# Optimization experiments

Hardware: AMD Instinct MI355X
Metric: run time of the kernel (lower is better)

Reference implementation:

```python
import jax, jax.numpy as jnp
import numpy as np

BIG = 1e9
GRAPH_LAYERS = 2
FLOW_ITERS = 10
DUAL_ITERS = 10
STEP = 0.1
MOM = 0.9


def _forward(node_features, node_embeddings, demands, adj, neighborhoods,
             enc_W0, enc_b0, enc_W1, enc_b1,
             attn_W, attn_a_src, attn_a_dst, nbr_q,
             gru_W, gru_U, gru_b,
             dec_W0, dec_b0, dec_W1, dec_b1,
             dual_W0, dual_b0, dual_W1, dual_b1):
    E = enc_W1.shape[1]
    K = neighborhoods.shape[0]
    # --- node encoder MLP (tanh, activate_final=True) ---
    x = jnp.concatenate([node_embeddings, node_features], axis=-1)  # [B,N,Fin]
    h = jnp.tanh(jnp.tanh(x @ enc_W0 + enc_b0) @ enc_W1 + enc_b1)   # [B,N,E]
    attn_coefs = None
    for _ in range(GRAPH_LAYERS):
        # --- AttentionNeighborhood: multi-head GAT per hop level, then attention over levels ---
        z = jnp.einsum('bnd,hde->hbne', h, attn_W)                   # [H,B,N,E]
        s_src = jnp.einsum('hbne,he->hbn', z, attn_a_src)
        s_dst = jnp.einsum('hbne,he->hbn', z, attn_a_dst)
        scores = jnp.tanh(s_src[:, :, :, None] + s_dst[:, :, None, :])  # [H,B,N,N]
        aggs = []
        for k in range(K):
            masked = jnp.where(neighborhoods[k][None] > 0, scores, -BIG)
            alpha = jax.nn.softmax(masked, axis=-1)                  # [H,B,N,N]
            agg = jnp.tanh(jnp.einsum('hbnm,hbme->hbne', alpha, z).mean(axis=0))  # heads averaged -> [B,N,E]
            aggs.append(agg)
        aggs = jnp.stack(aggs, axis=2)                               # [B,N,K,E]
        attn_coefs = jax.nn.softmax(jnp.tanh(jnp.einsum('bnke,e->bnk', aggs, nbr_q)), axis=-1)
        nxt = jnp.einsum('bnk,bnke->bne', attn_coefs, aggs)          # [B,N,E]
        # --- GRU state update (tanh activation) ---
        zr = jax.nn.sigmoid(nxt @ gru_W[:, :2 * E] + h @ gru_U[:, :2 * E] + gru_b[:2 * E])
        zg, r = zr[..., :E], zr[..., E:]
        h_tilde = jnp.tanh(nxt @ gru_W[:, 2 * E:] + (r * h) @ gru_U[:, 2 * E:] + gru_b[2 * E:])
        h = (1.0 - zg) * h + zg * h_tilde
    # --- flow-proportion decoder + masked softmax over neighbors ---
    node_weights = jnp.tanh(h @ dec_W0 + dec_b0) @ dec_W1 + dec_b1   # [B,N,1]
    pred = adj * jnp.swapaxes(node_weights, 1, 2)                    # adj * node_weights^T
    weights = -BIG * (1.0 - adj) + pred
    prop = jax.nn.softmax(weights, axis=-1)                          # [B,N,N]
    # --- iterative min-cost-flow solver ---
    def mcf_step(flow, _):
        inflow = flow.sum(axis=1)[:, :, None]                        # inflow_i = sum_j flow[j,i]
        return prop * jax.nn.relu(inflow - demands), None
    flow, _ = jax.lax.scan(mcf_step, jnp.zeros_like(prop), None, length=FLOW_ITERS)
    # should_correct_flows: cancel opposing flow on each edge pair
    flow = flow - adj * jnp.minimum(flow, jnp.swapaxes(flow, 1, 2))
    flow_cost = jnp.sum(flow * flow, axis=(1, 2))                    # square cost, per graph
    # --- dual decoder + projected momentum ascent dual-flow solver ---
    dual_vars = jnp.tanh(h @ dual_W0 + dual_b0) @ dual_W1 + dual_b1  # [B,N,1]
    dual_diff = adj * (dual_vars - jnp.swapaxes(dual_vars, 1, 2))    # [B,N,N]
    def dual_step(carry, _):
        y, m = carry
        g = 2.0 * y - dual_diff                                      # d/dy [y^2 - dual_diff*y]
        m = MOM * m + g
        y = adj * jax.nn.relu(y - STEP * m)
        return (y, m), None
    (dflow, _m), _ = jax.lax.scan(dual_step,
                                  (jnp.zeros_like(dual_diff), jnp.zeros_like(dual_diff)),
                                  None, length=DUAL_ITERS)
    dual_demand = jnp.sum(dual_vars * demands, axis=(1, 2))
    dual_cost = jnp.sum(dflow * dflow - dual_diff * dflow, axis=(1, 2)) - dual_demand
    return flow_cost - dual_cost                                     # primal-dual gap loss, [B]


def setup_inputs() -> dict:
    key = jax.random.key(0)
    ks = jax.random.split(key, 24)
    B, N, Femb, Ffeat, E, H = 2, 2048, 16, 2, 64, 2
    Fin = Femb + Ffeat
    node_embeddings = jax.random.normal(ks[0], (B, N, Femb), jnp.float32)
    node_features = jax.random.normal(ks[1], (B, N, Ffeat), jnp.float32)
    d = jax.random.normal(ks[2], (B, N, 1), jnp.float32) * 0.1
    demands = d - d.mean(axis=1, keepdims=True)                      # balanced demands
    eye = jnp.eye(N, dtype=jnp.float32)
    u = jax.random.uniform(ks[3], (B, N, N))
    adj = (u < 0.008).astype(jnp.float32) * (1.0 - eye)              # avg degree ~16
    a2 = (jnp.matmul(adj, adj) > 0).astype(jnp.float32) * (1.0 - eye)
    neighborhoods = jnp.stack([adj, a2], axis=0)                     # [K,B,N,N]
    def init(k, fan_in, shape):
        return jax.random.normal(k, shape, jnp.float32) / jnp.sqrt(float(fan_in))
    return {
        'node_features': node_features, 'node_embeddings': node_embeddings,
        'demands': demands, 'adj': adj, 'neighborhoods': neighborhoods,
        'enc_W0': init(ks[4], Fin, (Fin, 64)), 'enc_b0': jnp.zeros((64,)),
        'enc_W1': init(ks[5], 64, (64, E)), 'enc_b1': jnp.zeros((E,)),
        'attn_W': init(ks[6], E, (H, E, E)),
        'attn_a_src': init(ks[7], E, (H, E)), 'attn_a_dst': init(ks[8], E, (H, E)),
        'nbr_q': init(ks[9], E, (E,)),
        'gru_W': init(ks[10], E, (E, 3 * E)), 'gru_U': init(ks[11], E, (E, 3 * E)),
        'gru_b': jnp.zeros((3 * E,)),
        'dec_W0': init(ks[12], E, (E, 64)), 'dec_b0': jnp.zeros((64,)),
        'dec_W1': init(ks[13], 64, (64, 1)), 'dec_b1': jnp.zeros((1,)),
        'dual_W0': init(ks[14], E, (E, 64)), 'dual_b0': jnp.zeros((64,)),
        'dual_W1': init(ks[15], 64, (64, 1)), 'dual_b1': jnp.zeros((1,)),
    }


def reference(node_features, node_embeddings, demands, adj, neighborhoods,
              enc_W0, enc_b0, enc_W1, enc_b1,
              attn_W, attn_a_src, attn_a_dst, nbr_q,
              gru_W, gru_U, gru_b,
              dec_W0, dec_b0, dec_W1, dec_b1,
              dual_W0, dual_b0, dual_W1, dual_b1):
    return _forward(node_features, node_embeddings, demands, adj, neighborhoods,
                    enc_W0, enc_b0, enc_W1, enc_b1,
                    attn_W, attn_a_src, attn_a_dst, nbr_q,
                    gru_W, gru_U, gru_b,
                    dec_W0, dec_b0, dec_W1, dec_b1,
                    dual_W0, dual_b0, dual_W1, dual_b1)
```

## Files before the change

kernel.cpp:

```cpp
#include <hip/hip_runtime.h>

#define B_ 2
#define N_ 2048
#define E_ 64
#define FIN_ 18
#define ADJ_CAP 128
#define A2_CAP 1024
#define ROWS 8

__device__ __forceinline__ float wave_sum(float v) {
  #pragma unroll
  for (int o = 32; o > 0; o >>= 1) v += __shfl_xor(v, o);
  return v;
}
__device__ __forceinline__ float wave_max(float v) {
  #pragma unroll
  for (int o = 32; o > 0; o >>= 1) v = fmaxf(v, __shfl_xor(v, o));
  return v;
}

__global__ void k_zero(int* __restrict__ tcnt, float* __restrict__ accum) {
  int i = blockIdx.x * 256 + threadIdx.x;
  if (i < B_ * N_) tcnt[i] = 0;
  if (i < 8) accum[i] = 0.f;
}

__global__ void k_csr(const float* __restrict__ nbhd, int* __restrict__ adj_idx,
                      int* __restrict__ adj_cnt, int* __restrict__ a2_idx,
                      int* __restrict__ a2_cnt) {
  int wid = blockIdx.x * 4 + (threadIdx.x >> 6);
  int lane = threadIdx.x & 63;
  int k = wid / (B_ * N_);
  int rem = wid - k * (B_ * N_);
  const float* row = nbhd + ((size_t)k * (B_ * N_) + rem) * N_;
  int cap = (k == 0) ? ADJ_CAP : A2_CAP;
  int* idx = ((k == 0) ? adj_idx : a2_idx) + (size_t)rem * cap;
  int* cntp = ((k == 0) ? adj_cnt : a2_cnt) + rem;
  int cnt = 0;
  for (int j0 = 0; j0 < N_; j0 += 64) {
    float v = row[j0 + lane];
    bool p = v > 0.f;
    unsigned long long m = __ballot(p);
    int pre = __popcll(m & ((1ull << lane) - 1ull));
    if (p) { int pos = cnt + pre; if (pos < cap) idx[pos] = j0 + lane; }
    cnt += __popcll(m);
  }
  if (lane == 0) *cntp = (cnt < cap) ? cnt : cap;
}

__global__ void k_enc(const float* __restrict__ emb, const float* __restrict__ feat,
                      const float* __restrict__ W0, const float* __restrict__ b0,
                      const float* __restrict__ W1, const float* __restrict__ b1,
                      float* __restrict__ h) {
  int j = threadIdx.x;
  int row0 = blockIdx.x * ROWS;
  __shared__ float X[ROWS][FIN_];
  __shared__ float HID[ROWS][64];
  for (int t = j; t < ROWS * FIN_; t += 64) {
    int r = t / FIN_, d = t % FIN_;
    int row = row0 + r;
    X[r][d] = (d < 16) ? emb[(size_t)row * 16 + d] : feat[(size_t)row * 2 + (d - 16)];
  }
  __syncthreads();
  float acc[ROWS];
  #pragma unroll
  for (int r = 0; r < ROWS; r++) acc[r] = b0[j];
  for (int d = 0; d < FIN_; d++) {
    float w = W0[d * 64 + j];
    #pragma unroll
    for (int r = 0; r < ROWS; r++) acc[r] += X[r][d] * w;
  }
  #pragma unroll
  for (int r = 0; r < ROWS; r++) HID[r][j] = tanhf(acc[r]);
  __syncthreads();
  float acc2[ROWS];
  #pragma unroll
  for (int r = 0; r < ROWS; r++) acc2[r] = b1[j];
  for (int d = 0; d < 64; d++) {
    float w = W1[d * 64 + j];
    #pragma unroll
    for (int r = 0; r < ROWS; r++) acc2[r] += HID[r][d] * w;
  }
  #pragma unroll
  for (int r = 0; r < ROWS; r++) h[(size_t)(row0 + r) * 64 + j] = tanhf(acc2[r]);
}

__global__ void k_z(const float* __restrict__ h, const float* __restrict__ attn_W,
                    const float* __restrict__ a_src, const float* __restrict__ a_dst,
                    float* __restrict__ z, float* __restrict__ ssrc, float* __restrict__ sdst) {
  int tid = threadIdx.x;
  int head = tid >> 6, j = tid & 63;
  int row0 = blockIdx.x * ROWS;
  __shared__ float HR[ROWS][64];
  for (int t = tid; t < ROWS * 64; t += 128) HR[t >> 6][t & 63] = h[(size_t)row0 * 64 + t];
  __syncthreads();
  float acc[ROWS];
  #pragma unroll
  for (int r = 0; r < ROWS; r++) acc[r] = 0.f;
  const float* W = attn_W + head * 64 * 64;
  for (int d = 0; d < 64; d++) {
    float w = W[d * 64 + j];
    #pragma unroll
    for (int r = 0; r < ROWS; r++) acc[r] += HR[r][d] * w;
  }
  float as = a_src[head * 64 + j], ad = a_dst[head * 64 + j];
  #pragma unroll
  for (int r = 0; r < ROWS; r++) {
    float zv = acc[r];
    z[((size_t)head * (B_ * N_) + row0 + r) * 64 + j] = zv;
    float rs = wave_sum(zv * as);
    float rd = wave_sum(zv * ad);
    if (j == 0) {
      ssrc[head * (B_ * N_) + row0 + r] = rs;
      sdst[head * (B_ * N_) + row0 + r] = rd;
    }
  }
}

__global__ void k_agg(const int* __restrict__ adj_idx, const int* __restrict__ adj_cnt,
                      const int* __restrict__ a2_idx, const int* __restrict__ a2_cnt,
                      const float* __restrict__ z, const float* __restrict__ ssrc,
                      const float* __restrict__ sdst, float* __restrict__ aggs) {
  int k = blockIdx.x & 1;
  int row = blockIdx.x >> 1;
  int tid = threadIdx.x;
  int w = tid >> 6, lane = tid & 63;
  int b = row >> 11;
  int cap = (k == 0) ? ADJ_CAP : A2_CAP;
  const int* idx = ((k == 0) ? adj_idx : a2_idx) + (size_t)row * cap;
  int cnt = ((k == 0) ? adj_cnt : a2_cnt)[row];
  __shared__ float SC0[A2_CAP], SC1[A2_CAP];
  __shared__ int COL[A2_CAP];
  __shared__ float WS[4][64];
  __shared__ float RED[2][4];
  float ss0 = ssrc[row], ss1 = ssrc[B_ * N_ + row];
  const float* sd0 = sdst + b * N_;
  const float* sd1 = sdst + B_ * N_ + b * N_;
  float sum0 = 0.f, sum1 = 0.f;
  for (int t = tid; t < cnt; t += 256) {
    int c = idx[t];
    COL[t] = c;
    float e0 = __expf(tanhf(ss0 + sd0[c]));
    float e1 = __expf(tanhf(ss1 + sd1[c]));
    SC0[t] = e0; SC1[t] = e1;
    sum0 += e0; sum1 += e1;
  }
  sum0 = wave_sum(sum0); sum1 = wave_sum(sum1);
  if (lane == 0) { RED[0][w] = sum0; RED[1][w] = sum1; }
  __syncthreads();
  float tot0 = RED[0][0] + RED[0][1] + RED[0][2] + RED[0][3];
  float tot1 = RED[1][0] + RED[1][1] + RED[1][2] + RED[1][3];
  float inv0 = (tot0 > 0.f) ? 1.f / tot0 : 0.f;
  float inv1 = (tot1 > 0.f) ? 1.f / tot1 : 0.f;
  const float* z0 = z + ((size_t)b * N_) * 64;
  const float* z1 = z + ((size_t)(B_ * N_) + b * N_) * 64;
  int g = lane >> 4, li = lane & 15;
  float4 a0 = {0.f, 0.f, 0.f, 0.f}, a1 = {0.f, 0.f, 0.f, 0.f};
  for (int base = w * 4; base < cnt; base += 16) {
    int t = base + g;
    if (t < cnt) {
      int c = COL[t];
      float e0 = SC0[t], e1 = SC1[t];
      float4 v0 = ((const float4*)(z0 + (size_t)c * 64))[li];
      float4 v1 = ((const float4*)(z1 + (size_t)c * 64))[li];
      a0.x += e0 * v0.x; a0.y += e0 * v0.y; a0.z += e0 * v0.z; a0.w += e0 * v0.w;
      a1.x += e1 * v1.x; a1.y += e1 * v1.y; a1.z += e1 * v1.z; a1.w += e1 * v1.w;
    }
  }
  #pragma unroll
  for (int o = 16; o <= 32; o <<= 1) {
    a0.x += __shfl_xor(a0.x, o); a0.y += __shfl_xor(a0.y, o);
    a0.z += __shfl_xor(a0.z, o); a0.w += __shfl_xor(a0.w, o);
    a1.x += __shfl_xor(a1.x, o); a1.y += __shfl_xor(a1.y, o);
    a1.z += __shfl_xor(a1.z, o); a1.w += __shfl_xor(a1.w, o);
  }
  if (g == 0) {
    WS[w][li * 4 + 0] = a0.x * inv0 + a1.x * inv1;
    WS[w][li * 4 + 1] = a0.y * inv0 + a1.y * inv1;
    WS[w][li * 4 + 2] = a0.z * inv0 + a1.z * inv1;
    WS[w][li * 4 + 3] = a0.w * inv0 + a1.w * inv1;
  }
  __syncthreads();
  if (tid < 64) {
    float s = WS[0][tid] + WS[1][tid] + WS[2][tid] + WS[3][tid];
    aggs[((size_t)row * 2 + k) * 64 + tid] = tanhf(0.5f * s);
  }
}

__global__ void k_comb(const float* __restrict__ aggs, const float* __restrict__ nbr_q,
                       const float* __restrict__ gru_W, const float* __restrict__ gru_U,
                       const float* __restrict__ gru_b, float* __restrict__ h) {
  int tid = threadIdx.x;
  int w = tid >> 6, j = tid & 63;
  int row0 = blockIdx.x * ROWS;
  __shared__ float NXT[ROWS][64], HROW[ROWS][64], RG[ROWS][64], ZG[ROWS][64];
  for (int t = tid; t < ROWS * 64; t += 128) HROW[t >> 6][t & 63] = h[(size_t)row0 * 64 + t];
  float q = nbr_q[j];
  for (int r = w * (ROWS / 2); r < (w + 1) * (ROWS / 2); r++) {
    float a0 = aggs[((size_t)(row0 + r) * 2 + 0) * 64 + j];
    float a1 = aggs[((size_t)(row0 + r) * 2 + 1) * 64 + j];
    float t0 = tanhf(wave_sum(a0 * q));
    float t1 = tanhf(wave_sum(a1 * q));
    float mx = fmaxf(t0, t1);
    float e0 = __expf(t0 - mx), e1 = __expf(t1 - mx);
    float inv = 1.f / (e0 + e1);
    NXT[r][j] = (e0 * a0 + e1 * a1) * inv;
  }
  __syncthreads();
  {
    float acc[ROWS];
    #pragma unroll
    for (int r = 0; r < ROWS; r++) acc[r] = gru_b[tid];
    for (int d = 0; d < 64; d++) {
      float wW = gru_W[d * 192 + tid];
      float wU = gru_U[d * 192 + tid];
      #pragma unroll
      for (int r = 0; r < ROWS; r++) acc[r] += NXT[r][d] * wW + HROW[r][d] * wU;
    }
    #pragma unroll
    for (int r = 0; r < ROWS; r++) {
      float zr = 1.f / (1.f + __expf(-acc[r]));
      if (tid < 64) ZG[r][tid] = zr; else RG[r][tid - 64] = zr;
    }
  }
  __syncthreads();
  if (tid < 64) {
    int col = 128 + tid;
    float acc[ROWS];
    #pragma unroll
    for (int r = 0; r < ROWS; r++) acc[r] = gru_b[col];
    for (int d = 0; d < 64; d++) {
      float wW = gru_W[d * 192 + col];
      float wU = gru_U[d * 192 + col];
      #pragma unroll
      for (int r = 0; r < ROWS; r++) acc[r] += NXT[r][d] * wW + (RG[r][d] * HROW[r][d]) * wU;
    }
    #pragma unroll
    for (int r = 0; r < ROWS; r++) {
      float ht = tanhf(acc[r]);
      float zg = ZG[r][tid];
      h[(size_t)(row0 + r) * 64 + tid] = (1.f - zg) * HROW[r][tid] + zg * ht;
    }
  }
}

__global__ void k_dec(const float* __restrict__ h, const float* __restrict__ dW0,
                      const float* __restrict__ db0, const float* __restrict__ dW1,
                      const float* __restrict__ db1, const float* __restrict__ uW0,
                      const float* __restrict__ ub0, const float* __restrict__ uW1,
                      const float* __restrict__ ub1, const float* __restrict__ demands,
                      float* __restrict__ nw, float* __restrict__ dv, float* accum) {
  int j = threadIdx.x;
  int row0 = blockIdx.x * ROWS;
  __shared__ float HROW[ROWS][64];
  for (int t = j; t < ROWS * 64; t += 64) HROW[t >> 6][t & 63] = h[(size_t)row0 * 64 + t];
  __syncthreads();
  float hd[ROWS], hu[ROWS];
  #pragma unroll
  for (int r = 0; r < ROWS; r++) { hd[r] = db0[j]; hu[r] = ub0[j]; }
  for (int d = 0; d < 64; d++) {
    float w0 = dW0[d * 64 + j], u0 = uW0[d * 64 + j];
    #pragma unroll
    for (int r = 0; r < ROWS; r++) { hd[r] += HROW[r][d] * w0; hu[r] += HROW[r][d] * u0; }
  }
  float w1 = dW1[j], u1 = uW1[j];
  float ddl = 0.f;
  #pragma unroll
  for (int r = 0; r < ROWS; r++) {
    float a = wave_sum(tanhf(hd[r]) * w1);
    float bb = wave_sum(tanhf(hu[r]) * u1);
    if (j == 0) {
      int row = row0 + r;
      float nwv = a + db1[0], dvv = bb + ub1[0];
      nw[row] = nwv; dv[row] = dvv;
      ddl += dvv * demands[row];
    }
  }
  if (j == 0) atomicAdd(&accum[4 + (row0 >> 11)], ddl);
}

__global__ void k_prop(const int* __restrict__ adj_idx, const int* __restrict__ adj_cnt,
                       const float* __restrict__ nw, const float* __restrict__ demands,
                       float* __restrict__ Pval, float* __restrict__ sA) {
  int row = blockIdx.x;
  int lane = threadIdx.x;
  int b = row >> 11;
  int cnt = adj_cnt[row];
  const int* idx = adj_idx + (size_t)row * ADJ_CAP;
  int c0 = (lane < cnt) ? idx[lane] : -1;
  int c1 = (lane + 64 < cnt) ? idx[lane + 64] : -1;
  float v0 = (c0 >= 0) ? nw[b * N_ + c0] : -1e30f;
  float v1 = (c1 >= 0) ? nw[b * N_ + c1] : -1e30f;
  float m = wave_max(fmaxf(v0, v1));
  float e0 = (c0 >= 0) ? __expf(v0 - m) : 0.f;
  float e1 = (c1 >= 0) ? __expf(v1 - m) : 0.f;
  float s = wave_sum(e0 + e1);
  float inv = (s > 0.f) ? 1.f / s : 0.f;
  if (c0 >= 0) Pval[(size_t)row * ADJ_CAP + lane] = e0 * inv;
  if (c1 >= 0) Pval[(size_t)row * ADJ_CAP + lane + 64] = e1 * inv;
  if (lane == 0) sA[row] = fmaxf(-demands[row], 0.f);
}

__global__ void k_transpose(const int* __restrict__ adj_idx, const int* __restrict__ adj_cnt,
                            const float* __restrict__ Pval, int* __restrict__ tcnt,
                            int* __restrict__ tsrc, float* __restrict__ tval) {
  int row = blockIdx.x;
  int lane = threadIdx.x;
  int cnt = adj_cnt[row];
  int base = row & ~(N_ - 1);
  for (int t = lane; t < cnt; t += 64) {
    int j = adj_idx[(size_t)row * ADJ_CAP + t];
    int col = base + j;
    int pos = atomicAdd(&tcnt[col], 1);
    if (pos < ADJ_CAP) {
      tsrc[(size_t)col * ADJ_CAP + pos] = row;
      tval[(size_t)col * ADJ_CAP + pos] = Pval[(size_t)row * ADJ_CAP + t];
    }
  }
}

__global__ void k_mcf_iter(const int* __restrict__ tcnt, const int* __restrict__ tsrc,
                           const float* __restrict__ tval, const float* __restrict__ demands,
                           const float* __restrict__ s_in, float* __restrict__ s_out) {
  int j = blockIdx.x * 64 + threadIdx.x;
  int cnt = tcnt[j];
  const int* src = tsrc + (size_t)j * ADJ_CAP;
  const float* val = tval + (size_t)j * ADJ_CAP;
  float c = 0.f;
  #pragma unroll 4
  for (int t = 0; t < cnt; t++) c += val[t] * s_in[src[t]];
  s_out[j] = fmaxf(c - demands[j], 0.f);
}

__global__ void k_flowdual(const int* __restrict__ adj_idx, const int* __restrict__ adj_cnt,
                           const float* __restrict__ Pval, const float* __restrict__ s,
                           const float* __restrict__ dv, float* accum) {
  int tid = threadIdx.x;
  int lane = tid & 63, w = tid >> 6;
  int row0 = blockIdx.x * 8;
  float fc = 0.f, dc = 0.f;
  for (int rr = w; rr < 8; rr += 4) {
    int row = row0 + rr;
    int b = row >> 11, i = row & (N_ - 1);
    int cnt = adj_cnt[row];
    float si = s[row], dvi = dv[row];
    const int* idx = adj_idx + (size_t)row * ADJ_CAP;
    const float* pv = Pval + (size_t)row * ADJ_CAP;
    for (int t = lane; t < cnt; t += 64) {
      int j = idx[t];
      float f_ij = si * pv[t];
      const int* jidx = adj_idx + (size_t)(b * N_ + j) * ADJ_CAP;
      int jcnt = adj_cnt[b * N_ + j];
      int lo = 0, hi = jcnt, pos = -1;
      while (lo < hi) {
        int mid = (lo + hi) >> 1;
        int v = jidx[mid];
        if (v == i) { pos = mid; break; }
        if (v < i) lo = mid + 1; else hi = mid;
      }
      float f_ji = (pos >= 0) ? s[b * N_ + j] * Pval[(size_t)(b * N_ + j) * ADJ_CAP + pos] : 0.f;
      float fin = f_ij - fminf(f_ij, f_ji);
      fc += fin * fin;
      float dd = dvi - dv[b * N_ + j];
      float y = 0.f, m = 0.f;
      #pragma unroll
      for (int q = 0; q < 10; q++) {
        float g = 2.f * y - dd;
        m = 0.9f * m + g;
        y = fmaxf(y - 0.1f * m, 0.f);
      }
      dc += y * y - dd * y;
    }
  }
  fc = wave_sum(fc); dc = wave_sum(dc);
  __shared__ float FB[4], DB[4];
  if (lane == 0) { FB[w] = fc; DB[w] = dc; }
  __syncthreads();
  if (tid == 0) {
    int b = row0 >> 11;
    atomicAdd(&accum[b], FB[0] + FB[1] + FB[2] + FB[3]);
    atomicAdd(&accum[2 + b], DB[0] + DB[1] + DB[2] + DB[3]);
  }
}

__global__ void k_fin(const float* accum, float* out) {
  int b = threadIdx.x;
  if (b < B_) out[b] = accum[b] - accum[2 + b] + accum[4 + b];
}

extern "C" void kernel_launch(void* const* d_in, const int* in_sizes, int n_in,
                              void* d_out, int out_size, void* d_ws, size_t ws_size,
                              hipStream_t stream) {
  const float* feat    = (const float*)d_in[0];
  const float* emb     = (const float*)d_in[1];
  const float* demands = (const float*)d_in[2];
  const float* nbhd    = (const float*)d_in[4];
  const float* enc_W0  = (const float*)d_in[5];
  const float* enc_b0  = (const float*)d_in[6];
  const float* enc_W1  = (const float*)d_in[7];
  const float* enc_b1  = (const float*)d_in[8];
  const float* attn_W  = (const float*)d_in[9];
  const float* a_src   = (const float*)d_in[10];
  const float* a_dst   = (const float*)d_in[11];
  const float* nbr_q   = (const float*)d_in[12];
  const float* gru_W   = (const float*)d_in[13];
  const float* gru_U   = (const float*)d_in[14];
  const float* gru_b   = (const float*)d_in[15];
  const float* dec_W0  = (const float*)d_in[16];
  const float* dec_b0  = (const float*)d_in[17];
  const float* dec_W1  = (const float*)d_in[18];
  const float* dec_b1  = (const float*)d_in[19];
  const float* dual_W0 = (const float*)d_in[20];
  const float* dual_b0 = (const float*)d_in[21];
  const float* dual_W1 = (const float*)d_in[22];
  const float* dual_b1 = (const float*)d_in[23];
  float* out = (float*)d_out;

  char* ws = (char*)d_ws;
  size_t off = 0;
  auto alloc = [&](size_t bytes) { char* p = ws + off; off += (bytes + 255) & ~(size_t)255; return p; };
  int*   adj_idx = (int*)  alloc((size_t)B_ * N_ * ADJ_CAP * 4);
  int*   adj_cnt = (int*)  alloc((size_t)B_ * N_ * 4);
  int*   a2_idx  = (int*)  alloc((size_t)B_ * N_ * A2_CAP * 4);
  int*   a2_cnt  = (int*)  alloc((size_t)B_ * N_ * 4);
  float* h       = (float*)alloc((size_t)B_ * N_ * 64 * 4);
  float* z       = (float*)alloc((size_t)2 * B_ * N_ * 64 * 4);
  float* ssrc    = (float*)alloc((size_t)2 * B_ * N_ * 4);
  float* sdst    = (float*)alloc((size_t)2 * B_ * N_ * 4);
  float* aggs    = (float*)alloc((size_t)B_ * N_ * 2 * 64 * 4);
  float* nw      = (float*)alloc((size_t)B_ * N_ * 4);
  float* dv      = (float*)alloc((size_t)B_ * N_ * 4);
  float* Pval    = (float*)alloc((size_t)B_ * N_ * ADJ_CAP * 4);
  int*   tcnt    = (int*)  alloc((size_t)B_ * N_ * 4);
  int*   tsrc    = (int*)  alloc((size_t)B_ * N_ * ADJ_CAP * 4);
  float* tval    = (float*)alloc((size_t)B_ * N_ * ADJ_CAP * 4);
  float* sA      = (float*)alloc((size_t)B_ * N_ * 4);
  float* sB      = (float*)alloc((size_t)B_ * N_ * 4);
  float* accum   = (float*)alloc(8 * 4);

  k_zero<<<(B_ * N_ + 255) / 256, 256, 0, stream>>>(tcnt, accum);
  k_csr<<<(2 * B_ * N_) / 4, 256, 0, stream>>>(nbhd, adj_idx, adj_cnt, a2_idx, a2_cnt);
  k_enc<<<(B_ * N_) / ROWS, 64, 0, stream>>>(emb, feat, enc_W0, enc_b0, enc_W1, enc_b1, h);
  for (int layer = 0; layer < 2; layer++) {
    k_z<<<(B_ * N_) / ROWS, 128, 0, stream>>>(h, attn_W, a_src, a_dst, z, ssrc, sdst);
    k_agg<<<B_ * N_ * 2, 256, 0, stream>>>(adj_idx, adj_cnt, a2_idx, a2_cnt, z, ssrc, sdst, aggs);
    k_comb<<<(B_ * N_) / ROWS, 128, 0, stream>>>(aggs, nbr_q, gru_W, gru_U, gru_b, h);
  }
  k_dec<<<(B_ * N_) / ROWS, 64, 0, stream>>>(h, dec_W0, dec_b0, dec_W1, dec_b1,
                                             dual_W0, dual_b0, dual_W1, dual_b1,
                                             demands, nw, dv, accum);
  k_prop<<<B_ * N_, 64, 0, stream>>>(adj_idx, adj_cnt, nw, demands, Pval, sA);
  k_transpose<<<B_ * N_, 64, 0, stream>>>(adj_idx, adj_cnt, Pval, tcnt, tsrc, tval);
  for (int it = 0; it < 9; it++) {
    float* sin  = (it & 1) ? sB : sA;
    float* sout = (it & 1) ? sA : sB;
    k_mcf_iter<<<(B_ * N_) / 64, 64, 0, stream>>>(tcnt, tsrc, tval, demands, sin, sout);
  }
  k_flowdual<<<(B_ * N_) / 8, 256, 0, stream>>>(adj_idx, adj_cnt, Pval, sB, dv, accum);
  k_fin<<<1, 64, 0, stream>>>(accum, out);
}
```

Measured before the change: 454.4 us.

## Split aggregation per hop, vectorize CSR scan, fuse zeroing, retune flow-dual mapping

After: 416.3 us. 8.4% less time.

```diff
diff --git a/kernel.cpp b/kernel.cpp
--- a/kernel.cpp
+++ b/kernel.cpp
@@ -18,18 +18,20 @@
   for (int o = 32; o > 0; o >>= 1) v = fmaxf(v, __shfl_xor(v, o));
   return v;
 }
-
-__global__ void k_zero(int* __restrict__ tcnt, float* __restrict__ accum) {
-  int i = blockIdx.x * 256 + threadIdx.x;
-  if (i < B_ * N_) tcnt[i] = 0;
-  if (i < 8) accum[i] = 0.f;
+__device__ __forceinline__ void grp_reduce(float4& a) {
+  #pragma unroll
+  for (int o = 16; o <= 32; o <<= 1) {
+    a.x += __shfl_xor(a.x, o); a.y += __shfl_xor(a.y, o);
+    a.z += __shfl_xor(a.z, o); a.w += __shfl_xor(a.w, o);
+  }
 }
 
 __global__ void k_csr(const float* __restrict__ nbhd, int* __restrict__ adj_idx,
                       int* __restrict__ adj_cnt, int* __restrict__ a2_idx,
-                      int* __restrict__ a2_cnt) {
+                      int* __restrict__ a2_cnt, float* __restrict__ accum) {
   int wid = blockIdx.x * 4 + (threadIdx.x >> 6);
   int lane = threadIdx.x & 63;
+  if (wid == 0 && lane < 8) accum[lane] = 0.f;
   int k = wid / (B_ * N_);
   int rem = wid - k * (B_ * N_);
   const float* row = nbhd + ((size_t)k * (B_ * N_) + rem) * N_;
@@ -37,13 +39,20 @@
   int* idx = ((k == 0) ? adj_idx : a2_idx) + (size_t)rem * cap;
   int* cntp = ((k == 0) ? adj_cnt : a2_cnt) + rem;
   int cnt = 0;
-  for (int j0 = 0; j0 < N_; j0 += 64) {
-    float v = row[j0 + lane];
-    bool p = v > 0.f;
-    unsigned long long m = __ballot(p);
-    int pre = __popcll(m & ((1ull << lane) - 1ull));
-    if (p) { int pos = cnt + pre; if (pos < cap) idx[pos] = j0 + lane; }
-    cnt += __popcll(m);
+  unsigned long long below = (1ull << lane) - 1ull;
+  for (int j0 = 0; j0 < N_; j0 += 256) {
+    float4 v = ((const float4*)(row + j0))[lane];
+    bool p0 = v.x > 0.f, p1 = v.y > 0.f, p2 = v.z > 0.f, p3 = v.w > 0.f;
+    unsigned long long b0 = __ballot(p0), b1 = __ballot(p1),
+                       b2 = __ballot(p2), b3 = __ballot(p3);
+    int pos = cnt + __popcll(b0 & below) + __popcll(b1 & below) +
+              __popcll(b2 & below) + __popcll(b3 & below);
+    int base_j = j0 + lane * 4;
+    if (p0) { if (pos < cap) idx[pos] = base_j;     pos++; }
+    if (p1) { if (pos < cap) idx[pos] = base_j + 1; pos++; }
+    if (p2) { if (pos < cap) idx[pos] = base_j + 2; pos++; }
+    if (p3) { if (pos < cap) idx[pos] = base_j + 3; pos++; }
+    cnt += __popcll(b0) + __popcll(b1) + __popcll(b2) + __popcll(b3);
   }
   if (lane == 0) *cntp = (cnt < cap) ? cnt : cap;
 }
@@ -87,7 +96,7 @@
 
 __global__ void k_z(const float* __restrict__ h, const float* __restrict__ attn_W,
                     const float* __restrict__ a_src, const float* __restrict__ a_dst,
-                    float* __restrict__ z, float* __restrict__ ssrc, float* __restrict__ sdst) {
+                    float* __restrict__ z, float* __restrict__ ssrc2, float* __restrict__ sdst2) {
   int tid = threadIdx.x;
   int head = tid >> 6, j = tid & 63;
   int row0 = blockIdx.x * ROWS;
@@ -111,79 +120,142 @@
     float rs = wave_sum(zv * as);
     float rd = wave_sum(zv * ad);
     if (j == 0) {
-      ssrc[head * (B_ * N_) + row0 + r] = rs;
-      sdst[head * (B_ * N_) + row0 + r] = rd;
-    }
-  }
-}
-
-__global__ void k_agg(const int* __restrict__ adj_idx, const int* __restrict__ adj_cnt,
-                      const int* __restrict__ a2_idx, const int* __restrict__ a2_cnt,
-                      const float* __restrict__ z, const float* __restrict__ ssrc,
-                      const float* __restrict__ sdst, float* __restrict__ aggs) {
-  int k = blockIdx.x & 1;
-  int row = blockIdx.x >> 1;
-  int tid = threadIdx.x;
-  int w = tid >> 6, lane = tid & 63;
+      ssrc2[(size_t)(row0 + r) * 2 + head] = rs;
+      sdst2[(size_t)(row0 + r) * 2 + head] = rd;
+    }
+  }
+}
+
+__global__ __launch_bounds__(64) void k_agg_adj(
+    const int* __restrict__ adj_idx, const int* __restrict__ adj_cnt,
+    const float* __restrict__ z, const float* __restrict__ ssrc2,
+    const float* __restrict__ sdst2, float* __restrict__ aggs) {
+  int row = blockIdx.x;
+  int lane = threadIdx.x;
   int b = row >> 11;
-  int cap = (k == 0) ? ADJ_CAP : A2_CAP;
-  const int* idx = ((k == 0) ? adj_idx : a2_idx) + (size_t)row * cap;
-  int cnt = ((k == 0) ? adj_cnt : a2_cnt)[row];
-  __shared__ float SC0[A2_CAP], SC1[A2_CAP];
-  __shared__ int COL[A2_CAP];
-  __shared__ float WS[4][64];
-  __shared__ float RED[2][4];
-  float ss0 = ssrc[row], ss1 = ssrc[B_ * N_ + row];
-  const float* sd0 = sdst + b * N_;
-  const float* sd1 = sdst + B_ * N_ + b * N_;
-  float sum0 = 0.f, sum1 = 0.f;
-  for (int t = tid; t < cnt; t += 256) {
-    int c = idx[t];
-    COL[t] = c;
-    float e0 = __expf(tanhf(ss0 + sd0[c]));
-    float e1 = __expf(tanhf(ss1 + sd1[c]));
-    SC0[t] = e0; SC1[t] = e1;
-    sum0 += e0; sum1 += e1;
-  }
-  sum0 = wave_sum(sum0); sum1 = wave_sum(sum1);
-  if (lane == 0) { RED[0][w] = sum0; RED[1][w] = sum1; }
-  __syncthreads();
-  float tot0 = RED[0][0] + RED[0][1] + RED[0][2] + RED[0][3];
-  float tot1 = RED[1][0] + RED[1][1] + RED[1][2] + RED[1][3];
+  int cnt = adj_cnt[row];
+  const int* idx = adj_idx + (size_t)row * ADJ_CAP;
+  float2 ss = ((const float2*)ssrc2)[row];
+  const float2* sd = (const float2*)sdst2 + (size_t)b * N_;
+  int col0 = 0, col1 = 0;
+  float e00 = 0.f, e10 = 0.f, e01 = 0.f, e11 = 0.f;
+  if (lane < cnt) {
+    col0 = idx[lane]; float2 s = sd[col0];
+    e00 = __expf(tanhf(ss.x + s.x)); e10 = __expf(tanhf(ss.y + s.y));
+  }
+  if (lane + 64 < cnt) {
+    col1 = idx[lane + 64]; float2 s = sd[col1];
+    e01 = __expf(tanhf(ss.x + s.x)); e11 = __expf(tanhf(ss.y + s.y));
+  }
+  float tot0 = wave_sum(e00 + e01), tot1 = wave_sum(e10 + e11);
   float inv0 = (tot0 > 0.f) ? 1.f / tot0 : 0.f;
   float inv1 = (tot1 > 0.f) ? 1.f / tot1 : 0.f;
-  const float* z0 = z + ((size_t)b * N_) * 64;
+  const float* z0 = z + (size_t)b * N_ * 64;
   const float* z1 = z + ((size_t)(B_ * N_) + b * N_) * 64;
   int g = lane >> 4, li = lane & 15;
   float4 a0 = {0.f, 0.f, 0.f, 0.f}, a1 = {0.f, 0.f, 0.f, 0.f};
-  for (int base = w * 4; base < cnt; base += 16) {
-    int t = base + g;
-    if (t < cnt) {
-      int c = COL[t];
-      float e0 = SC0[t], e1 = SC1[t];
+  for (int j0 = 0; j0 < 64; j0 += 4) {
+    if (j0 >= cnt) break;
+    int j = j0 + g;
+    int c = __shfl(col0, j);
+    float e0 = __shfl(e00, j), e1 = __shfl(e10, j);
+    if (j < cnt) {
       float4 v0 = ((const float4*)(z0 + (size_t)c * 64))[li];
       float4 v1 = ((const float4*)(z1 + (size_t)c * 64))[li];
       a0.x += e0 * v0.x; a0.y += e0 * v0.y; a0.z += e0 * v0.z; a0.w += e0 * v0.w;
       a1.x += e1 * v1.x; a1.y += e1 * v1.y; a1.z += e1 * v1.z; a1.w += e1 * v1.w;
     }
   }
-  #pragma unroll
-  for (int o = 16; o <= 32; o <<= 1) {
-    a0.x += __shfl_xor(a0.x, o); a0.y += __shfl_xor(a0.y, o);
-    a0.z += __shfl_xor(a0.z, o); a0.w += __shfl_xor(a0.w, o);
-    a1.x += __shfl_xor(a1.x, o); a1.y += __shfl_xor(a1.y, o);
-    a1.z += __shfl_xor(a1.z, o); a1.w += __shfl_xor(a1.w, o);
-  }
+  if (cnt > 64) {
+    for (int j0 = 0; j0 < 64; j0 += 4) {
+      if (64 + j0 >= cnt) break;
+      int j = j0 + g;
+      int c = __shfl(col1, j);
+      float e0 = __shfl(e01, j), e1 = __shfl(e11, j);
+      if (64 + j < cnt) {
+        float4 v0 = ((const float4*)(z0 + (size_t)c * 64))[li];
+        float4 v1 = ((const float4*)(z1 + (size_t)c * 64))[li];
+        a0.x += e0 * v0.x; a0.y += e0 * v0.y; a0.z += e0 * v0.z; a0.w += e0 * v0.w;
+        a1.x += e1 * v1.x; a1.y += e1 * v1.y; a1.z += e1 * v1.z; a1.w += e1 * v1.w;
+      }
+    }
+  }
+  grp_reduce(a0); grp_reduce(a1);
   if (g == 0) {
-    WS[w][li * 4 + 0] = a0.x * inv0 + a1.x * inv1;
-    WS[w][li * 4 + 1] = a0.y * inv0 + a1.y * inv1;
-    WS[w][li * 4 + 2] = a0.z * inv0 + a1.z * inv1;
-    WS[w][li * 4 + 3] = a0.w * inv0 + a1.w * inv1;
+    float4 o;
+    o.x = tanhf(0.5f * (a0.x * inv0 + a1.x * inv1));
+    o.y = tanhf(0.5f * (a0.y * inv0 + a1.y * inv1));
+    o.z = tanhf(0.5f * (a0.z * inv0 + a1.z * inv1));
+    o.w = tanhf(0.5f * (a0.w * inv0 + a1.w * inv1));
+    ((float4*)(aggs + ((size_t)row * 2 + 0) * 64))[li] = o;
+  }
+}
+
+__global__ __launch_bounds__(256) void k_agg_a2(
+    const int* __restrict__ a2_idx, const int* __restrict__ a2_cnt,
+    const float* __restrict__ z, const float* __restrict__ ssrc2,
+    const float* __restrict__ sdst2, float* __restrict__ aggs) {
+  int row = blockIdx.x;
+  int tid = threadIdx.x;
+  int w = tid >> 6, lane = tid & 63;
+  int b = row >> 11;
+  int cnt = a2_cnt[row];
+  const int* idx = a2_idx + (size_t)row * A2_CAP;
+  float2 ss = ((const float2*)ssrc2)[row];
+  const float2* sd = (const float2*)sdst2 + (size_t)b * N_;
+  int colr[4]; float e0r[4], e1r[4];
+  float s0 = 0.f, s1 = 0.f;
+  #pragma unroll
+  for (int c = 0; c < 4; c++) {
+    int t = c * 256 + tid;
+    colr[c] = 0; e0r[c] = 0.f; e1r[c] = 0.f;
+    if (t < cnt) {
+      int cc = idx[t]; colr[c] = cc;
+      float2 s = sd[cc];
+      e0r[c] = __expf(tanhf(ss.x + s.x));
+      e1r[c] = __expf(tanhf(ss.y + s.y));
+      s0 += e0r[c]; s1 += e1r[c];
+    }
+  }
+  s0 = wave_sum(s0); s1 = wave_sum(s1);
+  __shared__ float RED[2][4];
+  __shared__ float WS0[4][64], WS1[4][64];
+  if (lane == 0) { RED[0][w] = s0; RED[1][w] = s1; }
+  const float* z0 = z + (size_t)b * N_ * 64;
+  const float* z1 = z + ((size_t)(B_ * N_) + b * N_) * 64;
+  int g = lane >> 4, li = lane & 15;
+  float4 a0 = {0.f, 0.f, 0.f, 0.f}, a1 = {0.f, 0.f, 0.f, 0.f};
+  #pragma unroll
+  for (int c = 0; c < 4; c++) {
+    int base = c * 256 + w * 64;
+    if (base >= cnt) break;
+    for (int j0 = 0; j0 < 64; j0 += 4) {
+      if (base + j0 >= cnt) break;
+      int j = j0 + g;
+      int col = __shfl(colr[c], j);
+      float e0 = __shfl(e0r[c], j), e1 = __shfl(e1r[c], j);
+      if (base + j < cnt) {
+        float4 v0 = ((const float4*)(z0 + (size_t)col * 64))[li];
+        float4 v1 = ((const float4*)(z1 + (size_t)col * 64))[li];
+        a0.x += e0 * v0.x; a0.y += e0 * v0.y; a0.z += e0 * v0.z; a0.w += e0 * v0.w;
+        a1.x += e1 * v1.x; a1.y += e1 * v1.y; a1.z += e1 * v1.z; a1.w += e1 * v1.w;
+      }
+    }
+  }
+  grp_reduce(a0); grp_reduce(a1);
+  if (g == 0) {
+    ((float4*)WS0[w])[li] = a0;
+    ((float4*)WS1[w])[li] = a1;
   }
   __syncthreads();
   if (tid < 64) {
-    float s = WS[0][tid] + WS[1][tid] + WS[2][tid] + WS[3][tid];
-    aggs[((size_t)row * 2 + k) * 64 + tid] = tanhf(0.5f * s);
+    float tot0 = RED[0][0] + RED[0][1] + RED[0][2] + RED[0][3];
+    float tot1 = RED[1][0] + RED[1][1] + RED[1][2] + RED[1][3];
+    float inv0 = (tot0 > 0.f) ? 1.f / tot0 : 0.f;
+    float inv1 = (tot1 > 0.f) ? 1.f / tot1 : 0.f;
+    float r0 = WS0[0][tid] + WS0[1][tid] + WS0[2][tid] + WS0[3][tid];
+    float r1 = WS1[0][tid] + WS1[1][tid] + WS1[2][tid] + WS1[3][tid];
+    aggs[((size_t)row * 2 + 1) * 64 + tid] = tanhf(0.5f * (r0 * inv0 + r1 * inv1));
   }
 }
 
@@ -281,7 +353,8 @@
 
 __global__ void k_prop(const int* __restrict__ adj_idx, const int* __restrict__ adj_cnt,
                        const float* __restrict__ nw, const float* __restrict__ demands,
-                       float* __restrict__ Pval, float* __restrict__ sA) {
+                       float* __restrict__ Pval, float* __restrict__ sA,
+                       int* __restrict__ tcnt) {
   int row = blockIdx.x;
   int lane = threadIdx.x;
   int b = row >> 11;
@@ -299,6 +372,7 @@
   if (c0 >= 0) Pval[(size_t)row * ADJ_CAP + lane] = e0 * inv;
   if (c1 >= 0) Pval[(size_t)row * ADJ_CAP + lane + 64] = e1 * inv;
   if (lane == 0) sA[row] = fmaxf(-demands[row], 0.f);
+  if (lane == 63) tcnt[row] = 0;
 }
 
 __global__ void k_transpose(const int* __restrict__ adj_idx, const int* __restrict__ adj_cnt,
@@ -327,59 +401,63 @@
   const int* src = tsrc + (size_t)j * ADJ_CAP;
   const float* val = tval + (size_t)j * ADJ_CAP;
   float c = 0.f;
-  #pragma unroll 4
-  for (int t = 0; t < cnt; t++) c += val[t] * s_in[src[t]];
+  int c4 = cnt >> 2;
+  for (int q = 0; q < c4; q++) {
+    int4 s4 = ((const int4*)src)[q];
+    float4 v4 = ((const float4*)val)[q];
+    c += v4.x * s_in[s4.x] + v4.y * s_in[s4.y] + v4.z * s_in[s4.z] + v4.w * s_in[s4.w];
+  }
+  for (int t = c4 * 4; t < cnt; t++) c += val[t] * s_in[src[t]];
   s_out[j] = fmaxf(c - demands[j], 0.f);
 }
 
-__global__ void k_flowdual(const int* __restrict__ adj_idx, const int* __restrict__ adj_cnt,
-                           const float* __restrict__ Pval, const float* __restrict__ s,
-                           const float* __restrict__ dv, float* accum) {
+__global__ __launch_bounds__(256) void k_flowdual(
+    const int* __restrict__ adj_idx, const int* __restrict__ adj_cnt,
+    const float* __restrict__ Pval, const float* __restrict__ s,
+    const float* __restrict__ dv, float* accum) {
   int tid = threadIdx.x;
   int lane = tid & 63, w = tid >> 6;
-  int row0 = blockIdx.x * 8;
+  int r16 = lane >> 4, e = lane & 15;
+  int row = blockIdx.x * 16 + w * 4 + r16;
+  int b = row >> 11, i = row & (N_ - 1);
+  int cnt = adj_cnt[row];
+  float si = s[row], dvi = dv[row];
+  const int* idx = adj_idx + (size_t)row * ADJ_CAP;
+  const float* pv = Pval + (size_t)row * ADJ_CAP;
   float fc = 0.f, dc = 0.f;
-  for (int rr = w; rr < 8; rr += 4) {
-    int row = row0 + rr;
-    int b = row >> 11, i = row & (N_ - 1);
-    int cnt = adj_cnt[row];
-    float si = s[row], dvi = dv[row];
-    const int* idx = adj_idx + (size_t)row * ADJ_CAP;
-    const float* pv = Pval + (size_t)row * ADJ_CAP;
-    for (int t = lane; t < cnt; t += 64) {
-      int j = idx[t];
-      float f_ij = si * pv[t];
-      const int* jidx = adj_idx + (size_t)(b * N_ + j) * ADJ_CAP;
-      int jcnt = adj_cnt[b * N_ + j];
-      int lo = 0, hi = jcnt, pos = -1;
-      while (lo < hi) {
-        int mid = (lo + hi) >> 1;
-        int v = jidx[mid];
-        if (v == i) { pos = mid; break; }
-        if (v < i) lo = mid + 1; else hi = mid;
-      }
-      float f_ji = (pos >= 0) ? s[b * N_ + j] * Pval[(size_t)(b * N_ + j) * ADJ_CAP + pos] : 0.f;
-      float fin = f_ij - fminf(f_ij, f_ji);
-      fc += fin * fin;
-      float dd = dvi - dv[b * N_ + j];
-      float y = 0.f, m = 0.f;
-      #pragma unroll
-      for (int q = 0; q < 10; q++) {
-        float g = 2.f * y - dd;
-        m = 0.9f * m + g;
-        y = fmaxf(y - 0.1f * m, 0.f);
-      }
-      dc += y * y - dd * y;
-    }
+  for (int t = e; t < cnt; t += 16) {
+    int j = idx[t];
+    float f_ij = si * pv[t];
+    const int* jidx = adj_idx + (size_t)(b * N_ + j) * ADJ_CAP;
+    int jcnt = adj_cnt[b * N_ + j];
+    int lo = 0, hi = jcnt, pos = -1;
+    while (lo < hi) {
+      int mid = (lo + hi) >> 1;
+      int v = jidx[mid];
+      if (v == i) { pos = mid; break; }
+      if (v < i) lo = mid + 1; else hi = mid;
+    }
+    float f_ji = (pos >= 0) ? s[b * N_ + j] * Pval[(size_t)(b * N_ + j) * ADJ_CAP + pos] : 0.f;
+    float fin = f_ij - fminf(f_ij, f_ji);
+    fc += fin * fin;
+    float dd = dvi - dv[b * N_ + j];
+    float y = 0.f, m = 0.f;
+    #pragma unroll
+    for (int q = 0; q < 10; q++) {
+      float g = 2.f * y - dd;
+      m = 0.9f * m + g;
+      y = fmaxf(y - 0.1f * m, 0.f);
+    }
+    dc += y * y - dd * y;
   }
   fc = wave_sum(fc); dc = wave_sum(dc);
   __shared__ float FB[4], DB[4];
   if (lane == 0) { FB[w] = fc; DB[w] = dc; }
   __syncthreads();
   if (tid == 0) {
-    int b = row0 >> 11;
-    atomicAdd(&accum[b], FB[0] + FB[1] + FB[2] + FB[3]);
-    atomicAdd(&accum[2 + b], DB[0] + DB[1] + DB[2] + DB[3]);
+    int bb = (blockIdx.x * 16) >> 11;
+    atomicAdd(&accum[bb], FB[0] + FB[1] + FB[2] + FB[3]);
+    atomicAdd(&accum[2 + bb], DB[0] + DB[1] + DB[2] + DB[3]);
   }
 }
 
@@ -425,8 +503,8 @@
   int*   a2_cnt  = (int*)  alloc((size_t)B_ * N_ * 4);
   float* h       = (float*)alloc((size_t)B_ * N_ * 64 * 4);
   float* z       = (float*)alloc((size_t)2 * B_ * N_ * 64 * 4);
-  float* ssrc    = (float*)alloc((size_t)2 * B_ * N_ * 4);
-  float* sdst    = (float*)alloc((size_t)2 * B_ * N_ * 4);
+  float* ssrc2   = (float*)alloc((size_t)2 * B_ * N_ * 4);
+  float* sdst2   = (float*)alloc((size_t)2 * B_ * N_ * 4);
   float* aggs    = (float*)alloc((size_t)B_ * N_ * 2 * 64 * 4);
   float* nw      = (float*)alloc((size_t)B_ * N_ * 4);
   float* dv      = (float*)alloc((size_t)B_ * N_ * 4);
@@ -438,24 +516,24 @@
   float* sB      = (float*)alloc((size_t)B_ * N_ * 4);
   float* accum   = (float*)alloc(8 * 4);
 
-  k_zero<<<(B_ * N_ + 255) / 256, 256, 0, stream>>>(tcnt, accum);
-  k_csr<<<(2 * B_ * N_) / 4, 256, 0, stream>>>(nbhd, adj_idx, adj_cnt, a2_idx, a2_cnt);
+  k_csr<<<(2 * B_ * N_) / 4, 256, 0, stream>>>(nbhd, adj_idx, adj_cnt, a2_idx, a2_cnt, accum);
   k_enc<<<(B_ * N_) / ROWS, 64, 0, stream>>>(emb, feat, enc_W0, enc_b0, enc_W1, enc_b1, h);
   for (int layer = 0; layer < 2; layer++) {
-    k_z<<<(B_ * N_) / ROWS, 128, 0, stream>>>(h, attn_W, a_src, a_dst, z, ssrc, sdst);
-    k_agg<<<B_ * N_ * 2, 256, 0, stream>>>(adj_idx, adj_cnt, a2_idx, a2_cnt, z, ssrc, sdst, aggs);
+    k_z<<<(B_ * N_) / ROWS, 128, 0, stream>>>(h, attn_W, a_src, a_dst, z, ssrc2, sdst2);
+    k_agg_adj<<<B_ * N_, 64, 0, stream>>>(adj_idx, adj_cnt, z, ssrc2, sdst2, aggs);
+    k_agg_a2<<<B_ * N_, 256, 0, stream>>>(a2_idx, a2_cnt, z, ssrc2, sdst2, aggs);
     k_comb<<<(B_ * N_) / ROWS, 128, 0, stream>>>(aggs, nbr_q, gru_W, gru_U, gru_b, h);
   }
   k_dec<<<(B_ * N_) / ROWS, 64, 0, stream>>>(h, dec_W0, dec_b0, dec_W1, dec_b1,
                                              dual_W0, dual_b0, dual_W1, dual_b1,
                                              demands, nw, dv, accum);
-  k_prop<<<B_ * N_, 64, 0, stream>>>(adj_idx, adj_cnt, nw, demands, Pval, sA);
+  k_prop<<<B_ * N_, 64, 0, stream>>>(adj_idx, adj_cnt, nw, demands, Pval, sA, tcnt);
   k_transpose<<<B_ * N_, 64, 0, stream>>>(adj_idx, adj_cnt, Pval, tcnt, tsrc, tval);
   for (int it = 0; it < 9; it++) {
     float* sin  = (it & 1) ? sB : sA;
     float* sout = (it & 1) ? sA : sB;
     k_mcf_iter<<<(B_ * N_) / 64, 64, 0, stream>>>(tcnt, tsrc, tval, demands, sin, sout);
   }
-  k_flowdual<<<(B_ * N_) / 8, 256, 0, stream>>>(adj_idx, adj_cnt, Pval, sB, dv, accum);
+  k_flowdual<<<(B_ * N_) / 16, 256, 0, stream>>>(adj_idx, adj_cnt, Pval, sB, dv, accum);
   k_fin<<<1, 64, 0, stream>>>(accum, out);
 }
```
